# Optimization experiments

Measured on AMD Instinct MI355X. Metric: run time of the kernel, lower is better.

## Reference

```python
import jax, jax.numpy as jnp
import numpy as np

# AFD = permute -> VSSBlock (LN + SS2D Mamba selective scan, residual) -> permute
#       -> x + SAFM(ChannelLayerNorm(x))
C = 64        # in_channels (d_model)
DI = 128      # d_inner = expand(2) * d_model
N = 16        # d_state
R = 4         # dt_rank = ceil(64/16)
K = 4         # scan directions
LN_EPS = 1e-5
CN_EPS = 1e-6
B_, H_, W_ = 8, 64, 64


def setup_inputs() -> dict:
    key = jax.random.key(0)
    ks = jax.random.split(key, 16)
    f = lambda k, s, sc=0.02: jax.random.normal(k, s, jnp.float32) * sc
    return {
        'x': jax.random.normal(ks[0], (B_, C, H_, W_), jnp.float32),
        # VSSBlock ln_1
        'ln1_g': jnp.ones((C,), jnp.float32),
        'ln1_b': jnp.zeros((C,), jnp.float32),
        # SS2D
        'in_proj_w': f(ks[1], (2 * DI, C)),
        'in_proj_b': jnp.zeros((2 * DI,), jnp.float32),
        'conv_w': f(ks[2], (DI, 3, 3)),          # depthwise 3x3
        'conv_b': jnp.zeros((DI,), jnp.float32),
        'xproj_w': f(ks[3], (K, R + 2 * N, DI)),
        'dtproj_w': f(ks[4], (K, DI, R), 0.1),
        'dtproj_b': f(ks[5], (K, DI), 0.1),
        'A_logs': jnp.tile(jnp.log(jnp.arange(1, N + 1, dtype=jnp.float32)), (K * DI, 1)),
        'Ds': jnp.ones((K * DI,), jnp.float32),
        'outnorm_g': jnp.ones((DI,), jnp.float32),
        'outnorm_b': jnp.zeros((DI,), jnp.float32),
        'outproj_w': f(ks[6], (C, DI)),
        'outproj_b': jnp.zeros((C,), jnp.float32),
        # SAFM
        'mfr_w': f(ks[7], (4, C // 4, 3, 3)),    # 4 depthwise 3x3 convs
        'mfr_b': jnp.zeros((4, C // 4), jnp.float32),
        'aggr_w': f(ks[8], (C, C)),              # 1x1 conv
        'aggr_b': jnp.zeros((C,), jnp.float32),
        # channel LayerNorm (SAFMN-style, channels_first)
        'cn_g': jnp.ones((C,), jnp.float32),
        'cn_b': jnp.zeros((C,), jnp.float32),
    }


def _ln(x, g, b, eps):
    u = jnp.mean(x, -1, keepdims=True)
    v = jnp.mean((x - u) ** 2, -1, keepdims=True)
    return (x - u) * jax.lax.rsqrt(v + eps) * g + b


def _channel_ln(x, g, b):  # x: (B,C,H,W), normalize over C
    u = jnp.mean(x, 1, keepdims=True)
    v = jnp.mean((x - u) ** 2, 1, keepdims=True)
    return (x - u) * jax.lax.rsqrt(v + CN_EPS) * g[None, :, None, None] + b[None, :, None, None]


def _dwconv3(x, w, b):  # depthwise 3x3, pad 1. x: (B,C,H,W), w: (C,3,3)
    y = jax.lax.conv_general_dilated(x, w[:, None], (1, 1), 'SAME',
        dimension_numbers=('NCHW', 'OIHW', 'NCHW'), feature_group_count=x.shape[1])
    return y + b[None, :, None, None]


def _selective_scan(xs, dts, A, Bs, Cs, D):
    # xs,dts:(B,K,C,L)  Bs,Cs:(B,K,N,L)  A:(K,C,N)  D:(K,C)
    u = jnp.moveaxis(xs, -1, 0)
    dt = jnp.moveaxis(dts, -1, 0)
    Bl = jnp.moveaxis(Bs, -1, 0)
    Cl = jnp.moveaxis(Cs, -1, 0)

    def step(h, inp):
        u_t, dt_t, B_t, C_t = inp
        h = h * jnp.exp(dt_t[..., None] * A) + dt_t[..., None] * B_t[:, :, None, :] * u_t[..., None]
        return h, jnp.einsum('bkcn,bkn->bkc', h, C_t)

    h0 = jnp.zeros(u.shape[1:] + (A.shape[-1],), u.dtype)
    _, ys = jax.lax.scan(step, h0, (u, dt, Bl, Cl))
    return jnp.moveaxis(ys, 0, -1) + D[None, :, :, None] * xs


def _ss2d(x, in_proj_w, in_proj_b, conv_w, conv_b, xproj_w, dtproj_w, dtproj_b,
          A_logs, Ds, outnorm_g, outnorm_b, outproj_w, outproj_b):
    B, H, W, _ = x.shape
    L = H * W
    xz = jnp.einsum('bhwc,dc->bhwd', x, in_proj_w) + in_proj_b
    xi, z = jnp.split(xz, 2, axis=-1)
    xc = jnp.transpose(xi, (0, 3, 1, 2))                      # (B,DI,H,W)
    xc = jax.nn.silu(_dwconv3(xc, conv_w, conv_b))
    # 4-directional unfold: row-major, col-major, and their reverses
    x_flat = xc.reshape(B, DI, L)
    x_t = jnp.transpose(xc, (0, 1, 3, 2)).reshape(B, DI, L)
    x_hwwh = jnp.stack([x_flat, x_t], axis=1)                 # (B,2,DI,L)
    xs = jnp.concatenate([x_hwwh, jnp.flip(x_hwwh, axis=-1)], axis=1)  # (B,4,DI,L)
    x_dbl = jnp.einsum('bkdl,kcd->bkcl', xs, xproj_w)
    dts, Bs, Cs = jnp.split(x_dbl, [R, R + N], axis=2)
    dts = jnp.einsum('bkrl,kdr->bkdl', dts, dtproj_w)
    dts = jax.nn.softplus(dts + dtproj_b[None, :, :, None])
    A = -jnp.exp(A_logs).reshape(K, DI, N)
    out_y = _selective_scan(xs, dts, A, Bs, Cs, Ds.reshape(K, DI))  # (B,4,DI,L)
    inv = jnp.flip(out_y[:, 2:4], axis=-1)
    wh = jnp.transpose(out_y[:, 1].reshape(B, DI, W, H), (0, 1, 3, 2)).reshape(B, DI, L)
    invwh = jnp.transpose(inv[:, 1].reshape(B, DI, W, H), (0, 1, 3, 2)).reshape(B, DI, L)
    y = out_y[:, 0] + inv[:, 0] + wh + invwh                  # (B,DI,L)
    y = jnp.transpose(y, (0, 2, 1)).reshape(B, H, W, DI)
    y = _ln(y, outnorm_g, outnorm_b, LN_EPS) * jax.nn.silu(z)
    return jnp.einsum('bhwd,cd->bhwc', y, outproj_w) + outproj_b


def _safm(x, mfr_w, mfr_b, aggr_w, aggr_b):
    parts = jnp.split(x, 4, axis=1)
    outs = []
    for i in range(4):
        s = parts[i]
        k = 2 ** i
        if i > 0:  # adaptive max pool to (H/k, W/k) == maxpool k,k
            s = jax.lax.reduce_window(s, -jnp.inf, jax.lax.max, (1, 1, k, k), (1, 1, k, k), 'VALID')
        s = _dwconv3(s, mfr_w[i], mfr_b[i])
        if i > 0:  # nearest upsample back
            s = jnp.repeat(jnp.repeat(s, k, axis=2), k, axis=3)
        outs.append(s)
    out = jnp.concatenate(outs, axis=1)
    out = jnp.einsum('bchw,oc->bohw', out, aggr_w) + aggr_b[None, :, None, None]
    return jax.nn.gelu(out, approximate=False) * x


def reference(x, ln1_g, ln1_b, in_proj_w, in_proj_b, conv_w, conv_b, xproj_w,
              dtproj_w, dtproj_b, A_logs, Ds, outnorm_g, outnorm_b, outproj_w,
              outproj_b, mfr_w, mfr_b, aggr_w, aggr_b, cn_g, cn_b):
    xh = jnp.transpose(x, (0, 2, 3, 1))                       # NCHW -> NHWC
    xh = xh + _ss2d(_ln(xh, ln1_g, ln1_b, LN_EPS), in_proj_w, in_proj_b, conv_w,
                    conv_b, xproj_w, dtproj_w, dtproj_b, A_logs, Ds,
                    outnorm_g, outnorm_b, outproj_w, outproj_b)
    xo = jnp.transpose(xh, (0, 3, 1, 2))                      # NHWC -> NCHW
    return xo + _safm(_channel_ln(xo, cn_g, cn_b), mfr_w, mfr_b, aggr_w, aggr_b)
```

## Files before the change

kernel.cpp:

```cpp
#include <hip/hip_runtime.h>
#include <hip/hip_bf16.h>

#define BB 8
#define CC 64
#define HH 64
#define WW 64
#define LL 4096
#define DI 128
#define KK 4
#define NN 16
#define RR 4
#define XD 36
#define GG 64
#define TT 64

__device__ __forceinline__ float softplusf(float x){
    return fmaxf(x, 0.f) + __logf(1.f + __expf(-fabsf(x)));
}
__device__ __forceinline__ int p_of(int k, int t){
    int tt = (k & 2) ? (LL - 1 - t) : t;
    return (k & 1) ? ((tt & 63) * 64 + (tt >> 6)) : tt;
}

template<int CTRL>
__device__ __forceinline__ float dpp_xadd(float v){
    int t = __builtin_amdgcn_update_dpp(0, __float_as_int(v), CTRL, 0xF, 0xF, true);
    return v + __int_as_float(t);
}

__global__ __launch_bounds__(256) void k1_ln_inproj(
    const float* __restrict__ x,
    const float* __restrict__ ln1_g,
    const float* __restrict__ ln1_b,
    const float* __restrict__ ipw,
    const float* __restrict__ ipb,
    float* __restrict__ xi, float* __restrict__ zs)
{
    int bid = blockIdx.x;
    int b = bid >> 6, p0 = (bid & 63)*64;
    int tid = threadIdx.x;

    __shared__ float xs[64*65];
    __shared__ float lnxT[64*68];
    __shared__ float wT[16*260];
    __shared__ float gb[128];
    __shared__ float bias[256];
    __shared__ float red[512];
    __shared__ float mv[128];

    if (tid < 128) gb[tid] = (tid < 64) ? ln1_g[tid] : ln1_b[tid - 64];
    bias[tid] = ipb[tid];

    #pragma unroll
    for (int it = 0; it < 4; it++){
        int i = tid + it*256;
        int c = i >> 4, pq = i & 15;
        float4 v = *(const float4*)(x + ((size_t)(b*CC + c))*LL + p0 + pq*4);
        xs[(pq*4+0)*65 + c] = v.x;
        xs[(pq*4+1)*65 + c] = v.y;
        xs[(pq*4+2)*65 + c] = v.z;
        xs[(pq*4+3)*65 + c] = v.w;
    }
    __syncthreads();

    {
        int pix = tid >> 2, q = tid & 3;
        float s = 0.f, sq = 0.f;
        #pragma unroll
        for (int cc = 0; cc < 16; cc++){
            float v = xs[pix*65 + q*16 + cc];
            s += v; sq = fmaf(v, v, sq);
        }
        red[tid*2] = s; red[tid*2+1] = sq;
    }
    __syncthreads();
    if (tid < 64){
        float s = red[tid*8] + red[tid*8+2] + red[tid*8+4] + red[tid*8+6];
        float sq = red[tid*8+1] + red[tid*8+3] + red[tid*8+5] + red[tid*8+7];
        float mean = s * (1.f/64.f);
        float var  = sq * (1.f/64.f) - mean*mean;
        mv[tid*2] = mean; mv[tid*2+1] = rsqrtf(var + 1e-5f);
    }
    __syncthreads();
    {
        int pix = tid >> 2, q = tid & 3;
        float mean = mv[pix*2], rstd = mv[pix*2+1];
        #pragma unroll
        for (int cc = 0; cc < 16; cc++){
            int c = q*16 + cc;
            float v = (xs[pix*65 + c] - mean)*rstd*gb[c] + gb[64+c];
            lnxT[c*68 + pix] = v;
        }
    }

    int pt = tid >> 4, ot = tid & 15;
    float acc[16][4];
    #pragma unroll
    for (int j = 0; j < 16; j++)
        #pragma unroll
        for (int i2 = 0; i2 < 4; i2++) acc[j][i2] = 0.f;

    for (int kc = 0; kc < 4; kc++){
        __syncthreads();
        #pragma unroll
        for (int it = 0; it < 4; it++){
            int i = tid + it*256;
            int d = i >> 2, jq = i & 3;
            float4 wv = *(const float4*)(ipw + d*64 + kc*16 + jq*4);
            wT[(jq*4+0)*260 + d] = wv.x;
            wT[(jq*4+1)*260 + d] = wv.y;
            wT[(jq*4+2)*260 + d] = wv.z;
            wT[(jq*4+3)*260 + d] = wv.w;
        }
        __syncthreads();
        #pragma unroll
        for (int k = 0; k < 16; k++){
            float4 rv = *(const float4*)(lnxT + (kc*16 + k)*68 + pt*4);
            #pragma unroll
            for (int g = 0; g < 4; g++){
                float4 wv = *(const float4*)(wT + k*260 + g*64 + ot*4);
                acc[g*4+0][0] = fmaf(wv.x, rv.x, acc[g*4+0][0]);
                acc[g*4+0][1] = fmaf(wv.x, rv.y, acc[g*4+0][1]);
                acc[g*4+0][2] = fmaf(wv.x, rv.z, acc[g*4+0][2]);
                acc[g*4+0][3] = fmaf(wv.x, rv.w, acc[g*4+0][3]);
                acc[g*4+1][0] = fmaf(wv.y, rv.x, acc[g*4+1][0]);
                acc[g*4+1][1] = fmaf(wv.y, rv.y, acc[g*4+1][1]);
                acc[g*4+1][2] = fmaf(wv.y, rv.z, acc[g*4+1][2]);
                acc[g*4+1][3] = fmaf(wv.y, rv.w, acc[g*4+1][3]);
                acc[g*4+2][0] = fmaf(wv.z, rv.x, acc[g*4+2][0]);
                acc[g*4+2][1] = fmaf(wv.z, rv.y, acc[g*4+2][1]);
                acc[g*4+2][2] = fmaf(wv.z, rv.z, acc[g*4+2][2]);
                acc[g*4+2][3] = fmaf(wv.z, rv.w, acc[g*4+2][3]);
                acc[g*4+3][0] = fmaf(wv.w, rv.x, acc[g*4+3][0]);
                acc[g*4+3][1] = fmaf(wv.w, rv.y, acc[g*4+3][1]);
                acc[g*4+3][2] = fmaf(wv.w, rv.z, acc[g*4+3][2]);
                acc[g*4+3][3] = fmaf(wv.w, rv.w, acc[g*4+3][3]);
            }
        }
    }

    #pragma unroll
    for (int i2 = 0; i2 < 4; i2++){
        size_t prow = ((size_t)(b*LL) + p0 + pt*4 + i2);
        #pragma unroll
        for (int g = 0; g < 4; g++){
            int dbase = g*64 + ot*4;
            float4 v;
            v.x = acc[g*4+0][i2] + bias[dbase+0];
            v.y = acc[g*4+1][i2] + bias[dbase+1];
            v.z = acc[g*4+2][i2] + bias[dbase+2];
            v.w = acc[g*4+3][i2] + bias[dbase+3];
            if (g < 2){
                *(float4*)(xi + prow*DI + dbase) = v;
            } else {
                v.x = v.x / (1.f + __expf(-v.x));
                v.y = v.y / (1.f + __expf(-v.y));
                v.z = v.z / (1.f + __expf(-v.z));
                v.w = v.w / (1.f + __expf(-v.w));
                *(float4*)(zs + prow*DI + dbase - 128) = v;
            }
        }
    }
}

__global__ __launch_bounds__(256) void k2_dwconv(
    const float* __restrict__ xi,
    const float* __restrict__ cw,
    const float* __restrict__ cb,
    float* __restrict__ xc)
{
    int idx = blockIdx.x*256 + threadIdx.x;
    int d = idx & 127;
    int bp = idx >> 7;
    int p = bp & 4095, b = bp >> 12;
    int h = p >> 6, w = p & 63;
    float acc = cb[d];
    #pragma unroll
    for (int ky = 0; ky < 3; ky++){
        int hh = h + ky - 1;
        if ((unsigned)hh >= 64u) continue;
        #pragma unroll
        for (int kx = 0; kx < 3; kx++){
            int ww = w + kx - 1;
            if ((unsigned)ww >= 64u) continue;
            acc = fmaf(xi[((size_t)(b*LL) + hh*64 + ww)*DI + d], cw[d*9 + ky*3 + kx], acc);
        }
    }
    float sg = 1.f / (1.f + __expf(-acc));
    xc[idx] = acc * sg;
}

__global__ __launch_bounds__(256) void k3_xdbl(
    const float* __restrict__ xc,
    const float* __restrict__ xpw,
    float* __restrict__ xdbl)
{
    int bid = blockIdx.x;
    int b = bid >> 6, ptile = bid & 63;
    int tid = threadIdx.x;
    int ot = tid & 15;
    int pt = tid >> 4;

    __shared__ float r[64*132];
    __shared__ float wT[32*192];

    const float* xcb = xc + ((size_t)(b*LL) + ptile*64)*DI;
    for (int i = tid; i < 2048; i += 256){
        int pix = i >> 5, kq = i & 31;
        float4 v = *(const float4*)(xcb + pix*128 + kq*4);
        *(float4*)(r + pix*132 + kq*4) = v;
    }

    float acc[9][4];
    #pragma unroll
    for (int j = 0; j < 9; j++)
        #pragma unroll
        for (int i2 = 0; i2 < 4; i2++) acc[j][i2] = 0.f;

    for (int kc = 0; kc < 4; kc++){
        __syncthreads();
        int k0 = kc*32;
        for (int i = tid; i < 1152; i += 256){
            int cl = i >> 3, jq = i & 7;
            float4 wv = *(const float4*)(xpw + cl*128 + k0 + jq*4);
            int o = (cl*456) >> 12;
            int j = cl - o*9;
            wT[(jq*4+0)*192 + o*12 + j] = wv.x;
            wT[(jq*4+1)*192 + o*12 + j] = wv.y;
            wT[(jq*4+2)*192 + o*12 + j] = wv.z;
            wT[(jq*4+3)*192 + o*12 + j] = wv.w;
        }
        __syncthreads();
        const float* rbase = r + (pt*4)*132 + k0;
        #pragma unroll 4
        for (int k = 0; k < 32; k++){
            float4 wa = *(const float4*)(wT + k*192 + ot*12);
            float4 wb = *(const float4*)(wT + k*192 + ot*12 + 4);
            float w8 = wT[k*192 + ot*12 + 8];
            float rv0 = rbase[k];
            float rv1 = rbase[132 + k];
            float rv2 = rbase[264 + k];
            float rv3 = rbase[396 + k];
            float wv[9] = {wa.x, wa.y, wa.z, wa.w, wb.x, wb.y, wb.z, wb.w, w8};
            float rv[4] = {rv0, rv1, rv2, rv3};
            #pragma unroll
            for (int j = 0; j < 9; j++)
                #pragma unroll
                for (int i2 = 0; i2 < 4; i2++)
                    acc[j][i2] = fmaf(wv[j], rv[i2], acc[j][i2]);
        }
    }

    int kd = ot >> 2;
    int cbase = (ot & 3)*9;
    size_t obase = ((size_t)(b*KK + kd))*LL;
    #pragma unroll
    for (int i2 = 0; i2 < 4; i2++){
        int p = ptile*64 + pt*4 + i2;
        int tT = (p & 63)*64 + (p >> 6);
        int t = (kd == 0) ? p : (kd == 1) ? tT : (kd == 2) ? (4095 - p) : (4095 - tT);
        float* dst = xdbl + (obase + t)*XD + cbase;
        #pragma unroll
        for (int j = 0; j < 9; j++) dst[j] = acc[j][i2];
    }
}

__global__ __launch_bounds__(128, 4) void k4a_local(
    const float* __restrict__ xc, const float* __restrict__ xdbl,
    const float* __restrict__ dtw, const float* __restrict__ dtb,
    const float* __restrict__ A_logs,
    float* __restrict__ Pbuf, float* __restrict__ Hbuf)
{
    int bid = blockIdx.x;
    int cc = bid & 63, k = (bid >> 6) & 3, b = bid >> 8;
    int d = threadIdx.x;
    int kd = k*DI + d;
    float4 wv4 = *(const float4*)(dtw + kd*4);
    float bias = dtb[kd];
    float An[16];
    {
        const float4* al = (const float4*)(A_logs + kd*16);
        #pragma unroll
        for (int i = 0; i < 4; i++){
            float4 a = al[i];
            An[i*4+0] = -__expf(a.x); An[i*4+1] = -__expf(a.y);
            An[i*4+2] = -__expf(a.z); An[i*4+3] = -__expf(a.w);
        }
    }
    __shared__ float sraw[TT*XD];
    const float* src = xdbl + ((size_t)(b*KK + k)*LL + cc*TT)*XD;
    for (int i = threadIdx.x; i < TT*XD/4; i += 128)
        ((float4*)sraw)[i] = ((const float4*)src)[i];
    __syncthreads();

    const float* xcb = xc + (size_t)b*LL*DI;
    float h[16];
    #pragma unroll
    for (int i = 0; i < 16; i++) h[i] = 0.f;
    float Sdt = 0.f;
    for (int t = 0; t < TT; t++){
        const float* rp = sraw + t*XD;
        float4 xr = *(const float4*)rp;
        float dtr = fmaf(xr.x, wv4.x, fmaf(xr.y, wv4.y, fmaf(xr.z, wv4.z, fmaf(xr.w, wv4.w, bias))));
        float dt = softplusf(dtr);
        Sdt += dt;
        int p = p_of(k, cc*TT + t);
        float u = xcb[(size_t)p*DI + d];
        float du = dt * u;
        float4 B0 = *(const float4*)(rp + 4);
        float4 B1 = *(const float4*)(rp + 8);
        float4 B2 = *(const float4*)(rp + 12);
        float4 B3 = *(const float4*)(rp + 16);
        float Bv[16] = {B0.x,B0.y,B0.z,B0.w, B1.x,B1.y,B1.z,B1.w,
                        B2.x,B2.y,B2.z,B2.w, B3.x,B3.y,B3.z,B3.w};
        #pragma unroll
        for (int i = 0; i < 16; i++){
            float e = __expf(dt * An[i]);
            h[i] = fmaf(h[i], e, du * Bv[i]);
        }
    }
    size_t ob = ((size_t)bid)*2048 + d*16;
    #pragma unroll
    for (int i = 0; i < 16; i++){
        Pbuf[ob + i] = __expf(An[i] * Sdt);
        Hbuf[ob + i] = h[i];
    }
}

__global__ __launch_bounds__(256) void k4b_prop(
    const float* __restrict__ Pbuf, const float* __restrict__ Hbuf,
    float* __restrict__ hin_buf)
{
    int chain = blockIdx.x*256 + threadIdx.x;
    int bk = chain >> 11, s = chain & 2047;
    float hin = 0.f;
    for (int c = 0; c < GG; c++){
        size_t idx = ((size_t)(bk*GG + c))*2048 + s;
        hin_buf[idx] = hin;
        hin = fmaf(Pbuf[idx], hin, Hbuf[idx]);
    }
}

__global__ __launch_bounds__(128, 4) void k4c_emit(
    const float* __restrict__ xc, const float* __restrict__ xdbl,
    const float* __restrict__ dtw, const float* __restrict__ dtb,
    const float* __restrict__ A_logs, const float* __restrict__ Ds,
    const float* __restrict__ hin_buf,
    float* __restrict__ y)
{
    int bid = blockIdx.x;
    int cc = bid & 63, k = (bid >> 6) & 3, b = bid >> 8;
    int d = threadIdx.x;
    int kd = k*DI + d;
    float4 wv4 = *(const float4*)(dtw + kd*4);
    float bias = dtb[kd];
    float Dv = Ds[kd];
    float An[16];
    {
        const float4* al = (const float4*)(A_logs + kd*16);
        #pragma unroll
        for (int i = 0; i < 4; i++){
            float4 a = al[i];
            An[i*4+0] = -__expf(a.x); An[i*4+1] = -__expf(a.y);
            An[i*4+2] = -__expf(a.z); An[i*4+3] = -__expf(a.w);
        }
    }
    __shared__ float sraw[TT*XD];
    const float* src = xdbl + ((size_t)(b*KK + k)*LL + cc*TT)*XD;
    for (int i = threadIdx.x; i < TT*XD/4; i += 128)
        ((float4*)sraw)[i] = ((const float4*)src)[i];
    __syncthreads();

    const float* xcb = xc + (size_t)b*LL*DI;
    float* yb = y + (size_t)b*LL*DI;
    float h[16];
    {
        const float4* hi = (const float4*)(hin_buf + ((size_t)bid)*2048 + d*16);
        #pragma unroll
        for (int i = 0; i < 4; i++){
            float4 a = hi[i];
            h[i*4+0] = a.x; h[i*4+1] = a.y; h[i*4+2] = a.z; h[i*4+3] = a.w;
        }
    }
    for (int t = 0; t < TT; t++){
        const float* rp = sraw + t*XD;
        float4 xr = *(const float4*)rp;
        float dtr = fmaf(xr.x, wv4.x, fmaf(xr.y, wv4.y, fmaf(xr.z, wv4.z, fmaf(xr.w, wv4.w, bias))));
        float dt = softplusf(dtr);
        int p = p_of(k, cc*TT + t);
        float u = xcb[(size_t)p*DI + d];
        float du = dt * u;
        float4 B0 = *(const float4*)(rp + 4);
        float4 B1 = *(const float4*)(rp + 8);
        float4 B2 = *(const float4*)(rp + 12);
        float4 B3 = *(const float4*)(rp + 16);
        float Bv[16] = {B0.x,B0.y,B0.z,B0.w, B1.x,B1.y,B1.z,B1.w,
                        B2.x,B2.y,B2.z,B2.w, B3.x,B3.y,B3.z,B3.w};
        float4 C0 = *(const float4*)(rp + 20);
        float4 C1 = *(const float4*)(rp + 24);
        float4 C2 = *(const float4*)(rp + 28);
        float4 C3 = *(const float4*)(rp + 32);
        float Cv[16] = {C0.x,C0.y,C0.z,C0.w, C1.x,C1.y,C1.z,C1.w,
                        C2.x,C2.y,C2.z,C2.w, C3.x,C3.y,C3.z,C3.w};
        float yv = Dv * u;
        #pragma unroll
        for (int i = 0; i < 16; i++){
            float e = __expf(dt * An[i]);
            h[i] = fmaf(h[i], e, du * Bv[i]);
            yv = fmaf(h[i], Cv[i], yv);
        }
        atomicAdd(&yb[(size_t)p*DI + d], yv);
    }
}

__global__ __launch_bounds__(256) void k4_scan(
    const float* __restrict__ xc, const float* __restrict__ xdbl,
    const float* __restrict__ dtw, const float* __restrict__ dtb,
    const float* __restrict__ A_logs, const float* __restrict__ Ds,
    float* __restrict__ y)
{
    int bid = blockIdx.x;
    int b = bid >> 5, k = (bid >> 3) & 3, grp = bid & 7;
    int d0 = grp * 16;
    int tid = threadIdx.x;
    int wv = tid >> 6, lane = tid & 63, n = lane & 15, j = lane >> 4;
    int ch = wv*4 + j;
    int d = d0 + ch;
    int kd = k*DI + d;
    float An = -__expf(A_logs[kd*NN + n]);
    int ch_s = tid & 15;
    int kds = k*DI + d0 + ch_s;
    float w0s = dtw[kds*4+0], w1s = dtw[kds*4+1], w2s = dtw[kds*4+2], w3s = dtw[kds*4+3];
    float bs  = dtb[kds];
    float Dvs = Ds[kds];
    __shared__ float sraw[64*XD];
    __shared__ float sdd[64*16*2];
    __shared__ float sdy[64*17];
    const float* xdbase = xdbl + (size_t)(b*KK + k)*LL*XD;
    const float* xcb = xc + (size_t)b*LL*DI;
    float* yb = y + (size_t)b*LL*DI;
    float h = 0.f;
    for (int cc = 0; cc < 64; cc++){
        __syncthreads();
        const float* src = xdbase + (size_t)cc*64*XD;
        for (int i2 = tid; i2 < 576; i2 += 256)
            ((float4*)sraw)[i2] = ((const float4*)src)[i2];
        #pragma unroll
        for (int it = 0; it < 4; it++){
            int idx = tid + it*256;
            int t = idx >> 4;
            int pu = p_of(k, cc*64 + t);
            float u = xcb[(size_t)pu*DI + d0 + ch_s];
            float4 xr = *(const float4*)(src + t*XD);
            float dtr = fmaf(xr.x, w0s, fmaf(xr.y, w1s, fmaf(xr.z, w2s, fmaf(xr.w, w3s, bs))));
            float dt = softplusf(dtr);
            sdd[idx*2]     = dt;
            sdd[idx*2 + 1] = dt*u;
            sdy[t*17 + ch_s] = Dvs * u;
        }
        __syncthreads();
        #pragma unroll
        for (int tg = 0; tg < 4; tg++){
            float myv = 0.f;
            #pragma unroll
            for (int it = 0; it < 16; it++){
                int t = tg*16 + it;
                float dt = sdd[(t*16 + ch)*2];
                float du = sdd[(t*16 + ch)*2 + 1];
                float Bn = sraw[t*XD + 4 + n];
                float Cn = sraw[t*XD + 20 + n];
                float e = __expf(dt * An);
                h = fmaf(h, e, du * Bn);
                float yv = h * Cn;
                yv = dpp_xadd<0xB1>(yv);
                yv = dpp_xadd<0x4E>(yv);
                yv = dpp_xadd<0x141>(yv);
                yv = dpp_xadd<0x140>(yv);
                if (it == n) myv = yv;
            }
            int t = tg*16 + n;
            float yt = myv + sdy[t*17 + ch];
            int p = p_of(k, cc*64 + t);
            atomicAdd(&yb[(size_t)p*DI + d], yt);
        }
    }
}

__global__ __launch_bounds__(256) void k5_out(
    const float* __restrict__ y, const float* __restrict__ zs,
    const float* __restrict__ on_g, const float* __restrict__ on_b,
    const float* __restrict__ opw,
    const float* __restrict__ opb,
    const float* __restrict__ x,
    float* __restrict__ xo)
{
    int bid = blockIdx.x;
    int b = bid >> 6, p0 = (bid & 63)*64;
    int tid = threadIdx.x;

    __shared__ float vT[128*68];
    __shared__ float wT[128*68];
    __shared__ float gb[256];
    __shared__ float ob[64];
    __shared__ float red[512];
    __shared__ float mv[128];

    gb[tid] = (tid < 128) ? on_g[tid] : on_b[tid - 128];
    if (tid < 64) ob[tid] = opb[tid];

    #pragma unroll
    for (int it = 0; it < 8; it++){
        int i = tid + it*256;
        int c = i >> 5, jq = i & 31;
        float4 wv = *(const float4*)(opw + c*128 + jq*4);
        wT[(jq*4+0)*68 + c] = wv.x;
        wT[(jq*4+1)*68 + c] = wv.y;
        wT[(jq*4+2)*68 + c] = wv.z;
        wT[(jq*4+3)*68 + c] = wv.w;
    }

    int pix = tid >> 2, q = tid & 3;
    size_t base = ((size_t)(b*LL) + p0 + pix)*DI + q*32;
    float yv[32];
    {
        const float4* y4 = (const float4*)(y + base);
        float s = 0.f, sq = 0.f;
        #pragma unroll
        for (int i = 0; i < 8; i++){
            float4 a = y4[i];
            yv[i*4+0] = a.x; yv[i*4+1] = a.y; yv[i*4+2] = a.z; yv[i*4+3] = a.w;
            s += a.x + a.y + a.z + a.w;
            sq = fmaf(a.x,a.x, fmaf(a.y,a.y, fmaf(a.z,a.z, fmaf(a.w,a.w, sq))));
        }
        red[tid*2] = s; red[tid*2+1] = sq;
    }
    __syncthreads();
    if (tid < 64){
        float s = red[tid*8] + red[tid*8+2] + red[tid*8+4] + red[tid*8+6];
        float sq = red[tid*8+1] + red[tid*8+3] + red[tid*8+5] + red[tid*8+7];
        float mean = s * (1.f/128.f);
        float var  = sq * (1.f/128.f) - mean*mean;
        mv[tid*2] = mean; mv[tid*2+1] = rsqrtf(var + 1e-5f);
    }
    __syncthreads();
    {
        float mean = mv[pix*2], rstd = mv[pix*2+1];
        const float4* z4 = (const float4*)(zs + base);
        #pragma unroll
        for (int i = 0; i < 8; i++){
            float4 zz = z4[i];
            float zv[4] = {zz.x, zz.y, zz.z, zz.w};
            #pragma unroll
            for (int jj = 0; jj < 4; jj++){
                int d = q*32 + i*4 + jj;
                float vn = (yv[i*4+jj] - mean)*rstd*gb[d] + gb[128+d];
                vT[d*68 + pix] = vn * zv[jj];
            }
        }
    }
    __syncthreads();

    int pt = tid >> 4, ot = tid & 15;
    float acc[4][4];
    #pragma unroll
    for (int j = 0; j < 4; j++)
        #pragma unroll
        for (int i2 = 0; i2 < 4; i2++) acc[j][i2] = 0.f;

    #pragma unroll 4
    for (int k = 0; k < 128; k++){
        float4 rv = *(const float4*)(vT + k*68 + pt*4);
        float4 wv = *(const float4*)(wT + k*68 + ot*4);
        acc[0][0] = fmaf(wv.x, rv.x, acc[0][0]); acc[0][1] = fmaf(wv.x, rv.y, acc[0][1]);
        acc[0][2] = fmaf(wv.x, rv.z, acc[0][2]); acc[0][3] = fmaf(wv.x, rv.w, acc[0][3]);
        acc[1][0] = fmaf(wv.y, rv.x, acc[1][0]); acc[1][1] = fmaf(wv.y, rv.y, acc[1][1]);
        acc[1][2] = fmaf(wv.y, rv.z, acc[1][2]); acc[1][3] = fmaf(wv.y, rv.w, acc[1][3]);
        acc[2][0] = fmaf(wv.z, rv.x, acc[2][0]); acc[2][1] = fmaf(wv.z, rv.y, acc[2][1]);
        acc[2][2] = fmaf(wv.z, rv.z, acc[2][2]); acc[2][3] = fmaf(wv.z, rv.w, acc[2][3]);
        acc[3][0] = fmaf(wv.w, rv.x, acc[3][0]); acc[3][1] = fmaf(wv.w, rv.y, acc[3][1]);
        acc[3][2] = fmaf(wv.w, rv.z, acc[3][2]); acc[3][3] = fmaf(wv.w, rv.w, acc[3][3]);
    }

    #pragma unroll
    for (int jj = 0; jj < 4; jj++){
        int c = ot*4 + jj;
        float4 xr = *(const float4*)(x + ((size_t)(b*CC + c))*LL + p0 + pt*4);
        acc[jj][0] += ob[c] + xr.x;
        acc[jj][1] += ob[c] + xr.y;
        acc[jj][2] += ob[c] + xr.z;
        acc[jj][3] += ob[c] + xr.w;
    }
    #pragma unroll
    for (int i2 = 0; i2 < 4; i2++){
        float4 v = make_float4(acc[0][i2], acc[1][i2], acc[2][i2], acc[3][i2]);
        *(float4*)(xo + ((size_t)(b*LL) + p0 + pt*4 + i2)*CC + ot*4) = v;
    }
}

__global__ __launch_bounds__(256) void k6_chln(
    const float* __restrict__ xo,
    const float* __restrict__ cn_g, const float* __restrict__ cn_b,
    float* __restrict__ cl)
{
    int t = blockIdx.x*256 + threadIdx.x;
    int pix = t >> 2, q = t & 3;
    const float4* r4 = (const float4*)(xo + (size_t)pix*CC + q*16);
    float4 a[4];
    float s = 0.f, sq = 0.f;
    #pragma unroll
    for (int i = 0; i < 4; i++){
        a[i] = r4[i];
        s += a[i].x + a[i].y + a[i].z + a[i].w;
        sq = fmaf(a[i].x,a[i].x, fmaf(a[i].y,a[i].y, fmaf(a[i].z,a[i].z, fmaf(a[i].w,a[i].w, sq))));
    }
    s += __shfl_xor(s, 1, 64);  sq += __shfl_xor(sq, 1, 64);
    s += __shfl_xor(s, 2, 64);  sq += __shfl_xor(sq, 2, 64);
    float mean = s * (1.f/64.f);
    float var  = sq * (1.f/64.f) - mean*mean;
    float rstd = rsqrtf(var + 1e-6f);
    const float4* g4 = (const float4*)(cn_g + q*16);
    const float4* b4 = (const float4*)(cn_b + q*16);
    float4* o4 = (float4*)(cl + (size_t)pix*CC + q*16);
    #pragma unroll
    for (int i = 0; i < 4; i++){
        float4 g = g4[i], bb = b4[i], r;
        r.x = (a[i].x - mean)*rstd*g.x + bb.x;
        r.y = (a[i].y - mean)*rstd*g.y + bb.y;
        r.z = (a[i].z - mean)*rstd*g.z + bb.z;
        r.w = (a[i].w - mean)*rstd*g.w + bb.w;
        o4[i] = r;
    }
}

__global__ __launch_bounds__(256) void k7_pools(const float* __restrict__ cl, float* __restrict__ pools)
{
    int idx = blockIdx.x*256 + threadIdx.x;
    int g, S, base;
    if (idx < 131072)      { g = 1; S = 32; base = 0; }
    else if (idx < 163840) { g = 2; S = 16; base = 131072; idx -= 131072; }
    else if (idx < 172032) { g = 3; S = 8;  base = 163840; idx -= 163840; }
    else return;
    int pw = idx % S; idx /= S;
    int ph = idx % S; idx /= S;
    int j = idx & 15; int b = idx >> 4;
    int kk = 64 / S;
    int c = g*16 + j;
    float m = -1e30f;
    for (int dy = 0; dy < kk; dy++)
        for (int dx = 0; dx < kk; dx++){
            int h = ph*kk + dy, w = pw*kk + dx;
            m = fmaxf(m, cl[((size_t)(b*LL) + h*64 + w)*CC + c]);
        }
    pools[base + ((size_t)(b*16 + j)*S + ph)*S + pw] = m;
}

__global__ __launch_bounds__(256) void k8_mfr(
    const float* __restrict__ cl, const float* __restrict__ pools,
    const float* __restrict__ mfr_w,
    const float* __restrict__ mfr_b,
    float* __restrict__ cat)
{
    int idx = blockIdx.x*256 + threadIdx.x;
    int c = idx & 63; int bp = idx >> 6;
    int p = bp & 4095, b = bp >> 12;
    int g = c >> 4, j = c & 15;
    int h = p >> 6, w = p & 63;
    float acc = mfr_b[g*16 + j];
    const float* wr = mfr_w + (g*16 + j)*9;
    if (g == 0){
        #pragma unroll
        for (int ky = 0; ky < 3; ky++){
            int hh = h + ky - 1; if ((unsigned)hh >= 64u) continue;
            #pragma unroll
            for (int kx = 0; kx < 3; kx++){
                int ww = w + kx - 1; if ((unsigned)ww >= 64u) continue;
                acc = fmaf(cl[((size_t)(b*LL) + hh*64 + ww)*CC + c], wr[ky*3 + kx], acc);
            }
        }
    } else {
        int S = 64 >> g;
        int ph = h >> g, pw = w >> g;
        int base = (g == 1) ? 0 : ((g == 2) ? 131072 : 163840);
        const float* P = pools + base + (size_t)(b*16 + j)*S*S;
        #pragma unroll
        for (int ky = 0; ky < 3; ky++){
            int hh = ph + ky - 1; if ((unsigned)hh >= (unsigned)S) continue;
            #pragma unroll
            for (int kx = 0; kx < 3; kx++){
                int ww = pw + kx - 1; if ((unsigned)ww >= (unsigned)S) continue;
                acc = fmaf(P[hh*S + ww], wr[ky*3 + kx], acc);
            }
        }
    }
    cat[idx] = acc;
}

__global__ __launch_bounds__(256) void k9_agg(
    const float* __restrict__ cat, const float* __restrict__ cl, const float* __restrict__ xo,
    const float* __restrict__ agw,
    const float* __restrict__ agb,
    float* __restrict__ out)
{
    int bid = blockIdx.x;
    int b = bid >> 6, p0 = (bid & 63)*64;
    int tid = threadIdx.x;

    __shared__ float catT[64*68];
    __shared__ float wT[64*68];
    __shared__ float ab[64];

    if (tid < 64) ab[tid] = agb[tid];
    #pragma unroll
    for (int it = 0; it < 4; it++){
        int i = tid + it*256;
        int pix = i >> 4, cq = i & 15;
        float4 v = *(const float4*)(cat + ((size_t)(b*LL) + p0 + pix)*CC + cq*4);
        catT[(cq*4+0)*68 + pix] = v.x;
        catT[(cq*4+1)*68 + pix] = v.y;
        catT[(cq*4+2)*68 + pix] = v.z;
        catT[(cq*4+3)*68 + pix] = v.w;
        int o = i >> 4;
        float4 wv = *(const float4*)(agw + o*64 + cq*4);
        wT[(cq*4+0)*68 + o] = wv.x;
        wT[(cq*4+1)*68 + o] = wv.y;
        wT[(cq*4+2)*68 + o] = wv.z;
        wT[(cq*4+3)*68 + o] = wv.w;
    }
    __syncthreads();

    int pt = tid >> 4, ot = tid & 15;
    float acc[4][4];
    #pragma unroll
    for (int j = 0; j < 4; j++)
        #pragma unroll
        for (int i2 = 0; i2 < 4; i2++) acc[j][i2] = 0.f;

    #pragma unroll 4
    for (int k = 0; k < 64; k++){
        float4 rv = *(const float4*)(catT + k*68 + pt*4);
        float4 wv = *(const float4*)(wT + k*68 + ot*4);
        acc[0][0] = fmaf(wv.x, rv.x, acc[0][0]); acc[0][1] = fmaf(wv.x, rv.y, acc[0][1]);
        acc[0][2] = fmaf(wv.x, rv.z, acc[0][2]); acc[0][3] = fmaf(wv.x, rv.w, acc[0][3]);
        acc[1][0] = fmaf(wv.y, rv.x, acc[1][0]); acc[1][1] = fmaf(wv.y, rv.y, acc[1][1]);
        acc[1][2] = fmaf(wv.y, rv.z, acc[1][2]); acc[1][3] = fmaf(wv.y, rv.w, acc[1][3]);
        acc[2][0] = fmaf(wv.z, rv.x, acc[2][0]); acc[2][1] = fmaf(wv.z, rv.y, acc[2][1]);
        acc[2][2] = fmaf(wv.z, rv.z, acc[2][2]); acc[2][3] = fmaf(wv.z, rv.w, acc[2][3]);
        acc[3][0] = fmaf(wv.w, rv.x, acc[3][0]); acc[3][1] = fmaf(wv.w, rv.y, acc[3][1]);
        acc[3][2] = fmaf(wv.w, rv.z, acc[3][2]); acc[3][3] = fmaf(wv.w, rv.w, acc[3][3]);
    }

    float res[4][4];
    #pragma unroll
    for (int i2 = 0; i2 < 4; i2++){
        size_t prow = ((size_t)(b*LL) + p0 + pt*4 + i2)*CC + ot*4;
        float4 clv = *(const float4*)(cl + prow);
        float4 xov = *(const float4*)(xo + prow);
        float cla[4] = {clv.x, clv.y, clv.z, clv.w};
        float xoa[4] = {xov.x, xov.y, xov.z, xov.w};
        #pragma unroll
        for (int jj = 0; jj < 4; jj++){
            float av = acc[jj][i2] + ab[ot*4 + jj];
            float gl = 0.5f*av*(1.f + erff(av*0.70710678118f));
            res[jj][i2] = xoa[jj] + gl*cla[jj];
        }
    }
    #pragma unroll
    for (int jj = 0; jj < 4; jj++){
        int o = ot*4 + jj;
        float4 v = make_float4(res[jj][0], res[jj][1], res[jj][2], res[jj][3]);
        *(float4*)(out + ((size_t)(b*CC + o))*LL + p0 + pt*4) = v;
    }
}

extern "C" void kernel_launch(void* const* d_in, const int* in_sizes, int n_in,
                              void* d_out, int out_size, void* d_ws, size_t ws_size,
                              hipStream_t stream)
{
    const float* x       = (const float*)d_in[0];
    const float* ln1_g   = (const float*)d_in[1];
    const float* ln1_b   = (const float*)d_in[2];
    const float* ipw     = (const float*)d_in[3];
    const float* ipb     = (const float*)d_in[4];
    const float* conv_w  = (const float*)d_in[5];
    const float* conv_b  = (const float*)d_in[6];
    const float* xpw     = (const float*)d_in[7];
    const float* dtw     = (const float*)d_in[8];
    const float* dtb     = (const float*)d_in[9];
    const float* A_logs  = (const float*)d_in[10];
    const float* Ds      = (const float*)d_in[11];
    const float* on_g    = (const float*)d_in[12];
    const float* on_b    = (const float*)d_in[13];
    const float* opw     = (const float*)d_in[14];
    const float* opb     = (const float*)d_in[15];
    const float* mfr_w   = (const float*)d_in[16];
    const float* mfr_b   = (const float*)d_in[17];
    const float* agw     = (const float*)d_in[18];
    const float* agb     = (const float*)d_in[19];
    const float* cn_g    = (const float*)d_in[20];
    const float* cn_b    = (const float*)d_in[21];
    float* out = (float*)d_out;

    float* ws = (float*)d_ws;
    float* xi    = ws;
    float* zs    = ws + 4194304;
    float* xc    = ws + 8388608;
    float* xdbl  = ws + 12582912;
    float* y     = xi;
    float* xo    = xc;
    float* pools = xc + 2097152;
    float* cl    = xdbl;
    float* cat   = zs;
    float* Pbuf  = ws + 17301504;
    float* Hbuf  = ws + 21495808;
    float* hinb  = ws + 25690112;
    bool par = ws_size >= (size_t)29884416 * 4;

    hipLaunchKernelGGL(k1_ln_inproj, dim3(BB*64), dim3(256), 0, stream,
                       x, ln1_g, ln1_b, ipw, ipb, xi, zs);
    hipLaunchKernelGGL(k2_dwconv, dim3(BB*LL*DI/256), dim3(256), 0, stream,
                       xi, conv_w, conv_b, xc);
    hipLaunchKernelGGL(k3_xdbl, dim3(BB*64), dim3(256), 0, stream,
                       xc, xpw, xdbl);
    hipMemsetAsync(y, 0, (size_t)BB*LL*DI*sizeof(float), stream);
    if (par){
        hipLaunchKernelGGL(k4a_local, dim3(BB*KK*GG), dim3(128), 0, stream,
                           xc, xdbl, dtw, dtb, A_logs, Pbuf, Hbuf);
        hipLaunchKernelGGL(k4b_prop, dim3(256), dim3(256), 0, stream,
                           Pbuf, Hbuf, hinb);
        hipLaunchKernelGGL(k4c_emit, dim3(BB*KK*GG), dim3(128), 0, stream,
                           xc, xdbl, dtw, dtb, A_logs, Ds, hinb, y);
    } else {
        hipLaunchKernelGGL(k4_scan, dim3(256), dim3(256), 0, stream,
                           xc, xdbl, dtw, dtb, A_logs, Ds, y);
    }
    hipLaunchKernelGGL(k5_out, dim3(BB*64), dim3(256), 0, stream,
                       y, zs, on_g, on_b, opw, opb, x, xo);
    hipLaunchKernelGGL(k6_chln, dim3(BB*LL*4/256), dim3(256), 0, stream,
                       xo, cn_g, cn_b, cl);
    hipLaunchKernelGGL(k7_pools, dim3((172032 + 255)/256), dim3(256), 0, stream,
                       cl, pools);
    hipLaunchKernelGGL(k8_mfr, dim3(BB*LL*CC/256), dim3(256), 0, stream,
                       cl, pools, mfr_w, mfr_b, cat);
    hipLaunchKernelGGL(k9_agg, dim3(BB*64), dim3(256), 0, stream,
                       cat, cl, xo, agw, agb, out);
}
```

Measured before the change: 423.5 us.

## Specialize scan exponentials for integer A, tile dwconv, fuse channel LN into out-proj

At runtime the scan kernels check whether the A values equal -(n+1). If they do, they compute exp(-dt) once and build exp(-n*dt) by repeated multiplication instead of issuing 16 exponentials per step. The depthwise conv now computes 4 adjacent pixels per thread, reusing the row loads and the hoisted weights. The channel LayerNorm is fused into the output-projection kernel, which removes one kernel launch and a full read of xo. The fast path depends on the A_logs initialization matching the test inputs, and the repeated products can accumulate rounding error.

```diff
diff --git a/kernel.cpp b/kernel.cpp
--- a/kernel.cpp
+++ b/kernel.cpp
@@ -171,23 +171,38 @@
 {
     int idx = blockIdx.x*256 + threadIdx.x;
     int d = idx & 127;
-    int bp = idx >> 7;
-    int p = bp & 4095, b = bp >> 12;
-    int h = p >> 6, w = p & 63;
-    float acc = cb[d];
+    int g = idx >> 7;
+    int p0 = (g & 1023) * 4;
+    int b = g >> 10;
+    int h = p0 >> 6, w0 = p0 & 63;
+    float wt[9];
+    #pragma unroll
+    for (int j = 0; j < 9; j++) wt[j] = cw[d*9 + j];
+    float bv = cb[d];
+    float acc[4] = {bv, bv, bv, bv};
     #pragma unroll
     for (int ky = 0; ky < 3; ky++){
         int hh = h + ky - 1;
         if ((unsigned)hh >= 64u) continue;
-        #pragma unroll
-        for (int kx = 0; kx < 3; kx++){
-            int ww = w + kx - 1;
-            if ((unsigned)ww >= 64u) continue;
-            acc = fmaf(xi[((size_t)(b*LL) + hh*64 + ww)*DI + d], cw[d*9 + ky*3 + kx], acc);
-        }
-    }
-    float sg = 1.f / (1.f + __expf(-acc));
-    xc[idx] = acc * sg;
+        const float* row = xi + ((size_t)(b*LL) + hh*64)*DI + d;
+        float v0 = (w0 > 0)  ? row[(w0-1)*DI] : 0.f;
+        float v1 = row[(w0+0)*DI];
+        float v2 = row[(w0+1)*DI];
+        float v3 = row[(w0+2)*DI];
+        float v4 = row[(w0+3)*DI];
+        float v5 = (w0 < 60) ? row[(w0+4)*DI] : 0.f;
+        float wa = wt[ky*3], wbv = wt[ky*3+1], wc = wt[ky*3+2];
+        acc[0] = fmaf(v0, wa, fmaf(v1, wbv, fmaf(v2, wc, acc[0])));
+        acc[1] = fmaf(v1, wa, fmaf(v2, wbv, fmaf(v3, wc, acc[1])));
+        acc[2] = fmaf(v2, wa, fmaf(v3, wbv, fmaf(v4, wc, acc[2])));
+        acc[3] = fmaf(v3, wa, fmaf(v4, wbv, fmaf(v5, wc, acc[3])));
+    }
+    #pragma unroll
+    for (int i = 0; i < 4; i++){
+        float a = acc[i];
+        float sg = 1.f / (1.f + __expf(-a));
+        xc[((size_t)(b*LL) + p0 + i)*DI + d] = a * sg;
+    }
 }
 
 __global__ __launch_bounds__(256) void k3_xdbl(
@@ -278,6 +293,7 @@
     float4 wv4 = *(const float4*)(dtw + kd*4);
     float bias = dtb[kd];
     float An[16];
+    bool fast = true;
     {
         const float4* al = (const float4*)(A_logs + kd*16);
         #pragma unroll
@@ -286,6 +302,9 @@
             An[i*4+0] = -__expf(a.x); An[i*4+1] = -__expf(a.y);
             An[i*4+2] = -__expf(a.z); An[i*4+3] = -__expf(a.w);
         }
+        #pragma unroll
+        for (int n = 0; n < 16; n++)
+            fast = fast && (fabsf(An[n] + (float)(n+1)) < 1e-3f*(float)(n+1));
     }
     __shared__ float sraw[TT*XD];
     const float* src = xdbl + ((size_t)(b*KK + k)*LL + cc*TT)*XD;
@@ -298,32 +317,71 @@
     #pragma unroll
     for (int i = 0; i < 16; i++) h[i] = 0.f;
     float Sdt = 0.f;
-    for (int t = 0; t < TT; t++){
-        const float* rp = sraw + t*XD;
-        float4 xr = *(const float4*)rp;
-        float dtr = fmaf(xr.x, wv4.x, fmaf(xr.y, wv4.y, fmaf(xr.z, wv4.z, fmaf(xr.w, wv4.w, bias))));
-        float dt = softplusf(dtr);
-        Sdt += dt;
-        int p = p_of(k, cc*TT + t);
-        float u = xcb[(size_t)p*DI + d];
-        float du = dt * u;
-        float4 B0 = *(const float4*)(rp + 4);
-        float4 B1 = *(const float4*)(rp + 8);
-        float4 B2 = *(const float4*)(rp + 12);
-        float4 B3 = *(const float4*)(rp + 16);
-        float Bv[16] = {B0.x,B0.y,B0.z,B0.w, B1.x,B1.y,B1.z,B1.w,
-                        B2.x,B2.y,B2.z,B2.w, B3.x,B3.y,B3.z,B3.w};
+
+    if (fast){
+        for (int t = 0; t < TT; t++){
+            const float* rp = sraw + t*XD;
+            float4 xr = *(const float4*)rp;
+            float dtr = fmaf(xr.x, wv4.x, fmaf(xr.y, wv4.y, fmaf(xr.z, wv4.z, fmaf(xr.w, wv4.w, bias))));
+            float dt = softplusf(dtr);
+            Sdt += dt;
+            int p = p_of(k, cc*TT + t);
+            float u = xcb[(size_t)p*DI + d];
+            float du = dt * u;
+            float4 B0 = *(const float4*)(rp + 4);
+            float4 B1 = *(const float4*)(rp + 8);
+            float4 B2 = *(const float4*)(rp + 12);
+            float4 B3 = *(const float4*)(rp + 16);
+            float Bv[16] = {B0.x,B0.y,B0.z,B0.w, B1.x,B1.y,B1.z,B1.w,
+                            B2.x,B2.y,B2.z,B2.w, B3.x,B3.y,B3.z,B3.w};
+            float e1 = exp2f(-1.44269504f * dt);
+            float e = e1;
+            h[0] = fmaf(h[0], e, du*Bv[0]);
+            #pragma unroll
+            for (int i = 1; i < 16; i++){
+                e *= e1;
+                h[i] = fmaf(h[i], e, du*Bv[i]);
+            }
+        }
+        size_t ob = ((size_t)bid)*2048 + d*16;
+        float P1 = exp2f(-1.44269504f * Sdt);
+        float P = P1;
+        Pbuf[ob] = P; Hbuf[ob] = h[0];
+        #pragma unroll
+        for (int i = 1; i < 16; i++){
+            P *= P1;
+            Pbuf[ob + i] = P;
+            Hbuf[ob + i] = h[i];
+        }
+    } else {
+        float An2[16];
+        #pragma unroll
+        for (int i = 0; i < 16; i++) An2[i] = An[i] * 1.44269504f;
+        for (int t = 0; t < TT; t++){
+            const float* rp = sraw + t*XD;
+            float4 xr = *(const float4*)rp;
+            float dtr = fmaf(xr.x, wv4.x, fmaf(xr.y, wv4.y, fmaf(xr.z, wv4.z, fmaf(xr.w, wv4.w, bias))));
+            float dt = softplusf(dtr);
+            Sdt += dt;
+            int p = p_of(k, cc*TT + t);
+            float u = xcb[(size_t)p*DI + d];
+            float du = dt * u;
+            float4 B0 = *(const float4*)(rp + 4);
+            float4 B1 = *(const float4*)(rp + 8);
+            float4 B2 = *(const float4*)(rp + 12);
+            float4 B3 = *(const float4*)(rp + 16);
+            float Bv[16] = {B0.x,B0.y,B0.z,B0.w, B1.x,B1.y,B1.z,B1.w,
+                            B2.x,B2.y,B2.z,B2.w, B3.x,B3.y,B3.z,B3.w};
+            #pragma unroll
+            for (int i = 0; i < 16; i++)
+                h[i] = fmaf(h[i], exp2f(dt*An2[i]), du*Bv[i]);
+        }
+        size_t ob = ((size_t)bid)*2048 + d*16;
         #pragma unroll
         for (int i = 0; i < 16; i++){
-            float e = __expf(dt * An[i]);
-            h[i] = fmaf(h[i], e, du * Bv[i]);
-        }
-    }
-    size_t ob = ((size_t)bid)*2048 + d*16;
-    #pragma unroll
-    for (int i = 0; i < 16; i++){
-        Pbuf[ob + i] = __expf(An[i] * Sdt);
-        Hbuf[ob + i] = h[i];
+            Pbuf[ob + i] = exp2f(An2[i] * Sdt);
+            Hbuf[ob + i] = h[i];
+        }
     }
 }
 
@@ -356,6 +414,7 @@
     float bias = dtb[kd];
     float Dv = Ds[kd];
     float An[16];
+    bool fast = true;
     {
         const float4* al = (const float4*)(A_logs + kd*16);
         #pragma unroll
@@ -364,6 +423,9 @@
             An[i*4+0] = -__expf(a.x); An[i*4+1] = -__expf(a.y);
             An[i*4+2] = -__expf(a.z); An[i*4+3] = -__expf(a.w);
         }
+        #pragma unroll
+        for (int n = 0; n < 16; n++)
+            fast = fast && (fabsf(An[n] + (float)(n+1)) < 1e-3f*(float)(n+1));
     }
     __shared__ float sraw[TT*XD];
     const float* src = xdbl + ((size_t)(b*KK + k)*LL + cc*TT)*XD;
@@ -382,34 +444,73 @@
             h[i*4+0] = a.x; h[i*4+1] = a.y; h[i*4+2] = a.z; h[i*4+3] = a.w;
         }
     }
-    for (int t = 0; t < TT; t++){
-        const float* rp = sraw + t*XD;
-        float4 xr = *(const float4*)rp;
-        float dtr = fmaf(xr.x, wv4.x, fmaf(xr.y, wv4.y, fmaf(xr.z, wv4.z, fmaf(xr.w, wv4.w, bias))));
-        float dt = softplusf(dtr);
-        int p = p_of(k, cc*TT + t);
-        float u = xcb[(size_t)p*DI + d];
-        float du = dt * u;
-        float4 B0 = *(const float4*)(rp + 4);
-        float4 B1 = *(const float4*)(rp + 8);
-        float4 B2 = *(const float4*)(rp + 12);
-        float4 B3 = *(const float4*)(rp + 16);
-        float Bv[16] = {B0.x,B0.y,B0.z,B0.w, B1.x,B1.y,B1.z,B1.w,
-                        B2.x,B2.y,B2.z,B2.w, B3.x,B3.y,B3.z,B3.w};
-        float4 C0 = *(const float4*)(rp + 20);
-        float4 C1 = *(const float4*)(rp + 24);
-        float4 C2 = *(const float4*)(rp + 28);
-        float4 C3 = *(const float4*)(rp + 32);
-        float Cv[16] = {C0.x,C0.y,C0.z,C0.w, C1.x,C1.y,C1.z,C1.w,
-                        C2.x,C2.y,C2.z,C2.w, C3.x,C3.y,C3.z,C3.w};
-        float yv = Dv * u;
-        #pragma unroll
-        for (int i = 0; i < 16; i++){
-            float e = __expf(dt * An[i]);
-            h[i] = fmaf(h[i], e, du * Bv[i]);
-            yv = fmaf(h[i], Cv[i], yv);
-        }
-        atomicAdd(&yb[(size_t)p*DI + d], yv);
+
+    if (fast){
+        for (int t = 0; t < TT; t++){
+            const float* rp = sraw + t*XD;
+            float4 xr = *(const float4*)rp;
+            float dtr = fmaf(xr.x, wv4.x, fmaf(xr.y, wv4.y, fmaf(xr.z, wv4.z, fmaf(xr.w, wv4.w, bias))));
+            float dt = softplusf(dtr);
+            int p = p_of(k, cc*TT + t);
+            float u = xcb[(size_t)p*DI + d];
+            float du = dt * u;
+            float4 B0 = *(const float4*)(rp + 4);
+            float4 B1 = *(const float4*)(rp + 8);
+            float4 B2 = *(const float4*)(rp + 12);
+            float4 B3 = *(const float4*)(rp + 16);
+            float Bv[16] = {B0.x,B0.y,B0.z,B0.w, B1.x,B1.y,B1.z,B1.w,
+                            B2.x,B2.y,B2.z,B2.w, B3.x,B3.y,B3.z,B3.w};
+            float4 C0 = *(const float4*)(rp + 20);
+            float4 C1 = *(const float4*)(rp + 24);
+            float4 C2 = *(const float4*)(rp + 28);
+            float4 C3 = *(const float4*)(rp + 32);
+            float Cv[16] = {C0.x,C0.y,C0.z,C0.w, C1.x,C1.y,C1.z,C1.w,
+                            C2.x,C2.y,C2.z,C2.w, C3.x,C3.y,C3.z,C3.w};
+            float yv = Dv * u;
+            float e1 = exp2f(-1.44269504f * dt);
+            float e = e1;
+            h[0] = fmaf(h[0], e, du*Bv[0]);
+            yv = fmaf(h[0], Cv[0], yv);
+            #pragma unroll
+            for (int i = 1; i < 16; i++){
+                e *= e1;
+                h[i] = fmaf(h[i], e, du*Bv[i]);
+                yv = fmaf(h[i], Cv[i], yv);
+            }
+            atomicAdd(&yb[(size_t)p*DI + d], yv);
+        }
+    } else {
+        float An2[16];
+        #pragma unroll
+        for (int i = 0; i < 16; i++) An2[i] = An[i] * 1.44269504f;
+        for (int t = 0; t < TT; t++){
+            const float* rp = sraw + t*XD;
+            float4 xr = *(const float4*)rp;
+            float dtr = fmaf(xr.x, wv4.x, fmaf(xr.y, wv4.y, fmaf(xr.z, wv4.z, fmaf(xr.w, wv4.w, bias))));
+            float dt = softplusf(dtr);
+            int p = p_of(k, cc*TT + t);
+            float u = xcb[(size_t)p*DI + d];
+            float du = dt * u;
+            float4 B0 = *(const float4*)(rp + 4);
+            float4 B1 = *(const float4*)(rp + 8);
+            float4 B2 = *(const float4*)(rp + 12);
+            float4 B3 = *(const float4*)(rp + 16);
+            float Bv[16] = {B0.x,B0.y,B0.z,B0.w, B1.x,B1.y,B1.z,B1.w,
+                            B2.x,B2.y,B2.z,B2.w, B3.x,B3.y,B3.z,B3.w};
+            float4 C0 = *(const float4*)(rp + 20);
+            float4 C1 = *(const float4*)(rp + 24);
+            float4 C2 = *(const float4*)(rp + 28);
+            float4 C3 = *(const float4*)(rp + 32);
+            float Cv[16] = {C0.x,C0.y,C0.z,C0.w, C1.x,C1.y,C1.z,C1.w,
+                            C2.x,C2.y,C2.z,C2.w, C3.x,C3.y,C3.z,C3.w};
+            float yv = Dv * u;
+            #pragma unroll
+            for (int i = 0; i < 16; i++){
+                h[i] = fmaf(h[i], exp2f(dt*An2[i]), du*Bv[i]);
+                yv = fmaf(h[i], Cv[i], yv);
+            }
+            atomicAdd(&yb[(size_t)p*DI + d], yv);
+        }
     }
 }
 
@@ -492,7 +593,8 @@
     const float* __restrict__ opw,
     const float* __restrict__ opb,
     const float* __restrict__ x,
-    float* __restrict__ xo)
+    const float* __restrict__ cn_g, const float* __restrict__ cn_b,
+    float* __restrict__ xo, float* __restrict__ cl)
 {
     int bid = blockIdx.x;
     int b = bid >> 6, p0 = (bid & 63)*64;
@@ -502,11 +604,13 @@
     __shared__ float wT[128*68];
     __shared__ float gb[256];
     __shared__ float ob[64];
-    __shared__ float red[512];
+    __shared__ float cgb[128];
+    __shared__ float red[2048];
     __shared__ float mv[128];
 
     gb[tid] = (tid < 128) ? on_g[tid] : on_b[tid - 128];
     if (tid < 64) ob[tid] = opb[tid];
+    if (tid >= 128 && tid < 256) cgb[tid-128] = (tid < 192) ? cn_g[tid-128] : cn_b[tid-192];
 
     #pragma unroll
     for (int it = 0; it < 8; it++){
@@ -552,9 +656,9 @@
             float zv[4] = {zz.x, zz.y, zz.z, zz.w};
             #pragma unroll
             for (int jj = 0; jj < 4; jj++){
-                int d = q*32 + i*4 + jj;
-                float vn = (yv[i*4+jj] - mean)*rstd*gb[d] + gb[128+d];
-                vT[d*68 + pix] = vn * zv[jj];
+                int dd = q*32 + i*4 + jj;
+                float vn = (yv[i*4+jj] - mean)*rstd*gb[dd] + gb[128+dd];
+                vT[dd*68 + pix] = vn * zv[jj];
             }
         }
     }
@@ -595,40 +699,38 @@
         float4 v = make_float4(acc[0][i2], acc[1][i2], acc[2][i2], acc[3][i2]);
         *(float4*)(xo + ((size_t)(b*LL) + p0 + pt*4 + i2)*CC + ot*4) = v;
     }
-}
-
-__global__ __launch_bounds__(256) void k6_chln(
-    const float* __restrict__ xo,
-    const float* __restrict__ cn_g, const float* __restrict__ cn_b,
-    float* __restrict__ cl)
-{
-    int t = blockIdx.x*256 + threadIdx.x;
-    int pix = t >> 2, q = t & 3;
-    const float4* r4 = (const float4*)(xo + (size_t)pix*CC + q*16);
-    float4 a[4];
-    float s = 0.f, sq = 0.f;
-    #pragma unroll
-    for (int i = 0; i < 4; i++){
-        a[i] = r4[i];
-        s += a[i].x + a[i].y + a[i].z + a[i].w;
-        sq = fmaf(a[i].x,a[i].x, fmaf(a[i].y,a[i].y, fmaf(a[i].z,a[i].z, fmaf(a[i].w,a[i].w, sq))));
-    }
-    s += __shfl_xor(s, 1, 64);  sq += __shfl_xor(sq, 1, 64);
-    s += __shfl_xor(s, 2, 64);  sq += __shfl_xor(sq, 2, 64);
-    float mean = s * (1.f/64.f);
-    float var  = sq * (1.f/64.f) - mean*mean;
-    float rstd = rsqrtf(var + 1e-6f);
-    const float4* g4 = (const float4*)(cn_g + q*16);
-    const float4* b4 = (const float4*)(cn_b + q*16);
-    float4* o4 = (float4*)(cl + (size_t)pix*CC + q*16);
-    #pragma unroll
-    for (int i = 0; i < 4; i++){
-        float4 g = g4[i], bb = b4[i], r;
-        r.x = (a[i].x - mean)*rstd*g.x + bb.x;
-        r.y = (a[i].y - mean)*rstd*g.y + bb.y;
-        r.z = (a[i].z - mean)*rstd*g.z + bb.z;
-        r.w = (a[i].w - mean)*rstd*g.w + bb.w;
-        o4[i] = r;
+
+    __syncthreads();
+    #pragma unroll
+    for (int i2 = 0; i2 < 4; i2++){
+        float s = acc[0][i2] + acc[1][i2] + acc[2][i2] + acc[3][i2];
+        float sq = fmaf(acc[0][i2],acc[0][i2], fmaf(acc[1][i2],acc[1][i2],
+                   fmaf(acc[2][i2],acc[2][i2], acc[3][i2]*acc[3][i2])));
+        red[(pt*4 + i2)*16 + ot] = s;
+        red[1024 + (pt*4 + i2)*16 + ot] = sq;
+    }
+    __syncthreads();
+    if (tid < 64){
+        float s = 0.f, sq = 0.f;
+        #pragma unroll
+        for (int o = 0; o < 16; o++){
+            s += red[tid*16 + o];
+            sq += red[1024 + tid*16 + o];
+        }
+        float mean = s * (1.f/64.f);
+        float var  = sq * (1.f/64.f) - mean*mean;
+        mv[tid*2] = mean; mv[tid*2+1] = rsqrtf(var + 1e-6f);
+    }
+    __syncthreads();
+    #pragma unroll
+    for (int i2 = 0; i2 < 4; i2++){
+        float mean = mv[(pt*4+i2)*2], rstd = mv[(pt*4+i2)*2+1];
+        float4 v;
+        v.x = (acc[0][i2] - mean)*rstd*cgb[ot*4+0] + cgb[64+ot*4+0];
+        v.y = (acc[1][i2] - mean)*rstd*cgb[ot*4+1] + cgb[64+ot*4+1];
+        v.z = (acc[2][i2] - mean)*rstd*cgb[ot*4+2] + cgb[64+ot*4+2];
+        v.w = (acc[3][i2] - mean)*rstd*cgb[ot*4+3] + cgb[64+ot*4+3];
+        *(float4*)(cl + ((size_t)(b*LL) + p0 + pt*4 + i2)*CC + ot*4) = v;
     }
 }
 
@@ -817,7 +919,7 @@
 
     hipLaunchKernelGGL(k1_ln_inproj, dim3(BB*64), dim3(256), 0, stream,
                        x, ln1_g, ln1_b, ipw, ipb, xi, zs);
-    hipLaunchKernelGGL(k2_dwconv, dim3(BB*LL*DI/256), dim3(256), 0, stream,
+    hipLaunchKernelGGL(k2_dwconv, dim3(BB*LL*DI/1024), dim3(256), 0, stream,
                        xi, conv_w, conv_b, xc);
     hipLaunchKernelGGL(k3_xdbl, dim3(BB*64), dim3(256), 0, stream,
                        xc, xpw, xdbl);
@@ -834,9 +936,7 @@
                            xc, xdbl, dtw, dtb, A_logs, Ds, y);
     }
     hipLaunchKernelGGL(k5_out, dim3(BB*64), dim3(256), 0, stream,
-                       y, zs, on_g, on_b, opw, opb, x, xo);
-    hipLaunchKernelGGL(k6_chln, dim3(BB*LL*4/256), dim3(256), 0, stream,
-                       xo, cn_g, cn_b, cl);
+                       y, zs, on_g, on_b, opw, opb, x, cn_g, cn_b, xo, cl);
     hipLaunchKernelGGL(k7_pools, dim3((172032 + 255)/256), dim3(256), 0, stream,
                        cl, pools);
     hipLaunchKernelGGL(k8_mfr, dim3(BB*LL*CC/256), dim3(256), 0, stream,
```

Measured after the change: 363.1 us. 1.17x faster.
